# Optimization experiments

Hardware: AMD Instinct MI355X
Metric: run time of the kernel (lower is better)

Reference implementation:

```python
import jax, jax.numpy as jnp
import numpy as np

B, T, C, H = 4, 4096, 1024, 64


def setup_inputs() -> dict:
    key = jax.random.key(0)
    kx, kk, kq, kv = jax.random.split(key, 4)
    x = jax.random.normal(kx, (B, T, C), dtype=jnp.float32)
    # bias-free linear weights, stored as [in, out] so y = x @ W
    Wk = jax.random.normal(kk, (C, H), dtype=jnp.float32) * (C ** -0.5)
    Wq = jax.random.normal(kq, (C, H), dtype=jnp.float32) * (C ** -0.5)
    Wv = jax.random.normal(kv, (C, H), dtype=jnp.float32) * (C ** -0.5)
    return {"x": x, "Wk": Wk, "Wq": Wq, "Wv": Wv}


def reference(x, Wk, Wq, Wv):
    b, t, c = x.shape
    k = x @ Wk  # [B,T,H]
    q = x @ Wq
    v = x @ Wv
    # NOTE: original scales by C**-0.5 (num_embed), not head_size**-0.5
    wei = jnp.einsum('bqh,bkh->bqk', q, k) * (c ** -0.5)  # [B,T,T]
    causal = jnp.tril(jnp.ones((t, t), dtype=bool))
    wei = jnp.where(causal, wei, -jnp.inf)
    wei = jax.nn.softmax(wei, axis=-1)
    # dropout p=0.0 (eval) -> identity
    return jnp.einsum('bqk,bkh->bqh', wei, v)  # [B,T,H]
```

## Files before the change

### kernel.cpp

```cpp
#include <hip/hip_runtime.h>
#include <hip/hip_bf16.h>

typedef unsigned short u16;
typedef unsigned int u32;
using f32x4 = __attribute__((ext_vector_type(4))) float;
using s16x8 = __attribute__((ext_vector_type(8))) short;

#define BATCH 4
#define SEQ   4096
#define CDIM  1024
#define HDIM  64
#define QT_N  256

__device__ inline u16 f32_to_bf16(float f) {
    __bf16 h = (__bf16)f;
    return __builtin_bit_cast(u16, h);
}
__device__ inline u32 pkbf16(float a, float b) {
    return (u32)f32_to_bf16(a) | ((u32)f32_to_bf16(b) << 16);
}
__device__ inline f32x4 mfma16(s16x8 a, s16x8 b, f32x4 c) {
    return __builtin_amdgcn_mfma_f32_16x16x32_bf16(a, b, c, 0, 0, 0);
}


__global__ __launch_bounds__(64) void wtrans_kernel(
        const float* __restrict__ Wk, const float* __restrict__ Wq,
        const float* __restrict__ Wv, u16* __restrict__ Wtf) {
    int bx = blockIdx.x;
    int nt = bx >> 5, kc = bx & 31;
    int lane = threadIdx.x;
    int l16 = lane & 15, qd = lane >> 4;
    int n = nt * 16 + l16;
    int a = n >> 6, h = n & 63;
    const float* src = (a == 0) ? Wk : (a == 1) ? Wq : Wv;
    float scale = (a == 1) ? 0.045084220027780106f : 1.0f;
    u32 p[4];
#pragma unroll
    for (int pp = 0; pp < 4; ++pp) {
        int k = kc * 32 + qd * 8 + pp * 2;
        p[pp] = pkbf16(src[k * HDIM + h] * scale, src[(k + 1) * HDIM + h] * scale);
    }
    uint4 u; u.x = p[0]; u.y = p[1]; u.z = p[2]; u.w = p[3];
    *(uint4*)&Wtf[(size_t)((nt * 32 + kc) * 64 + lane) * 8] = u;
}

__global__ __launch_bounds__(512, 4) void proj_kernel(
        const float* __restrict__ x, const u16* __restrict__ Wtf,
        u16* __restrict__ qf, u16* __restrict__ kf, u16* __restrict__ vf) {
    __shared__ __align__(16) u16 xs[32][1032];
    int t = threadIdx.x, lane = t & 63, w = t >> 6;
    int quad = lane >> 4, l16 = lane & 15;
    int row0 = blockIdx.x * 32;

    const float* xb = x + (size_t)row0 * CDIM;
#pragma unroll 4
    for (int i = 0; i < 8; ++i) {
        int flat = i * 4096 + t * 8;
        float4 f0 = *(const float4*)(xb + flat);
        float4 f1 = *(const float4*)(xb + flat + 4);
        uint4 u;
        u.x = pkbf16(f0.x, f0.y); u.y = pkbf16(f0.z, f0.w);
        u.z = pkbf16(f1.x, f1.y); u.w = pkbf16(f1.z, f1.w);
        *(uint4*)&xs[flat >> 10][flat & 1023] = u;
    }
    __syncthreads();

    f32x4 acc[3];
#pragma unroll
    for (int n = 0; n < 3; ++n) acc[n] = (f32x4){0.f, 0.f, 0.f, 0.f};

    int nt_lo = (3 * w) >> 1;
    const u16* bp0 = Wtf + ((size_t)(nt_lo * 32) * 64 + lane) * 8;
    const u16* bp1 = bp0 + (size_t)32 * 64 * 8;

    if ((w & 1) == 0) {
#pragma unroll 4
        for (int kc = 0; kc < 32; ++kc) {
            s16x8 a0 = *(const s16x8*)&xs[l16][kc * 32 + quad * 8];
            s16x8 a1 = *(const s16x8*)&xs[16 + l16][kc * 32 + quad * 8];
            s16x8 b0 = *(const s16x8*)(bp0 + (size_t)kc * 512);
            s16x8 b1 = *(const s16x8*)(bp1 + (size_t)kc * 512);
            acc[0] = mfma16(a0, b0, acc[0]);
            acc[1] = mfma16(a1, b0, acc[1]);
            acc[2] = mfma16(a0, b1, acc[2]);
        }
    } else {
#pragma unroll 4
        for (int kc = 0; kc < 32; ++kc) {
            s16x8 a0 = *(const s16x8*)&xs[l16][kc * 32 + quad * 8];
            s16x8 a1 = *(const s16x8*)&xs[16 + l16][kc * 32 + quad * 8];
            s16x8 b0 = *(const s16x8*)(bp0 + (size_t)kc * 512);
            s16x8 b1 = *(const s16x8*)(bp1 + (size_t)kc * 512);
            acc[0] = mfma16(a1, b0, acc[0]);
            acc[1] = mfma16(a0, b1, acc[1]);
            acc[2] = mfma16(a1, b1, acc[2]);
        }
    }

#pragma unroll
    for (int i = 0; i < 3; ++i) {
        int u = 3 * w + i;
        int nt = u >> 1, rh = u & 1;
        int n0 = nt * 16;
        int rbase = row0 + rh * 16 + quad * 4;
        int bb = rbase >> 12, rl = rbase & 4095;
        if (n0 < 128) {
            u16* dst = (n0 < 64) ? kf : qf;
            int h = (n0 & 63) + l16;
            int tt16 = rl >> 4, hc = h >> 5, qd2 = (h >> 3) & 3, j = h & 7;
            size_t base = ((size_t)((bb * 256 + tt16) * 2 + hc) * 64
                           + qd2 * 16 + (rl & 15)) * 8 + j;
#pragma unroll
            for (int r = 0; r < 4; ++r)
                dst[base + (size_t)r * 8] = f32_to_bf16(acc[i][r]);
        } else {
            int ht = (n0 - 128) >> 4;
            int kc2 = rl >> 5, qdv = (rl >> 3) & 3, j0 = rl & 7;
            u32 lo = pkbf16(acc[i][0], acc[i][1]);
            u32 hi = pkbf16(acc[i][2], acc[i][3]);
            size_t base = ((size_t)((bb * 128 + kc2) * 4 + ht) * 64
                           + qdv * 16 + l16) * 8 + j0;
            uint2 u2; u2.x = lo; u2.y = hi;
            *(uint2*)&vf[base] = u2;
        }
    }
}

__global__ __launch_bounds__(512, 4) void flash_kernel(
        const u16* __restrict__ qf, const u16* __restrict__ kf,
        const u16* __restrict__ vf, float* __restrict__ out) {
    __shared__ float cb[8][32][68];
    __shared__ float lb[8][32];
    int t = threadIdx.x, w = t >> 6, lane = t & 63;
    int quad = lane >> 4, l16 = lane & 15;
    int bx = blockIdx.x;
    int b = bx & 3;
    int j = (bx & 255) >> 2;
    int qt2 = (bx < 256) ? (127 - j) : j;

    const u16* qp0 = qf + ((size_t)((b * QT_N + qt2 * 2) * 2) * 64 + lane) * 8;
    const u16* qp1 = qp0 + 2 * 64 * 8;
    s16x8 bq[2][2];
    bq[0][0] = *(const s16x8*)qp0;
    bq[0][1] = *(const s16x8*)(qp0 + 512);
    bq[1][0] = *(const s16x8*)qp1;
    bq[1][1] = *(const s16x8*)(qp1 + 512);
    s16x8 ones;
#pragma unroll
    for (int jj = 0; jj < 8; ++jj) ones[jj] = (short)0x3F80;

    f32x4 o[2][4], o5[2];
#pragma unroll
    for (int tl = 0; tl < 2; ++tl) {
        o5[tl] = (f32x4){0.f, 0.f, 0.f, 0.f};
#pragma unroll
        for (int i = 0; i < 4; ++i) o[tl][i] = (f32x4){0.f, 0.f, 0.f, 0.f};
    }

    int nb = (qt2 * 32 + 32 + 63) >> 6;
    int iters = (nb + 7) >> 3;
    int rowq0 = qt2 * 32 + l16;
    const u16* kfb = kf + (size_t)b * 256 * 2 * 512;
    const u16* vfb = vf + (size_t)b * 128 * 4 * 512;
    int a0 = ((quad & 1) * 32 + l16) * 4;
    int a1 = a0 + 64;
    bool lotile = (quad < 2);

    auto iteration = [&](int kb, bool domask) {
        f32x4 sT[2][4];
#pragma unroll
        for (int kt = 0; kt < 4; ++kt) {
            const u16* kp = kfb + ((size_t)((kb * 4 + kt) * 2) * 64 + lane) * 8;
            s16x8 k0 = *(const s16x8*)kp;
            s16x8 k1 = *(const s16x8*)(kp + 512);
            f32x4 z = (f32x4){0.f, 0.f, 0.f, 0.f};
            sT[0][kt] = mfma16(k1, bq[0][1], mfma16(k0, bq[0][0], z));
            sT[1][kt] = mfma16(k1, bq[1][1], mfma16(k0, bq[1][0], z));
        }
        u32 P01[2][4], P23[2][4];
#pragma unroll
        for (int tl = 0; tl < 2; ++tl) {
            int rowq = rowq0 + tl * 16;
#pragma unroll
            for (int kt = 0; kt < 4; ++kt) {
                float e[4];
#pragma unroll
                for (int r = 0; r < 4; ++r) {
                    float ev = __builtin_amdgcn_exp2f(sT[tl][kt][r]);
                    if (domask) {
                        int key = kb * 64 + kt * 16 + quad * 4 + r;
                        ev = (key > rowq) ? 0.f : ev;
                    }
                    e[r] = ev;
                }
                P01[tl][kt] = pkbf16(e[0], e[1]);
                P23[tl][kt] = pkbf16(e[2], e[3]);
            }
        }
#pragma unroll
        for (int c = 0; c < 2; ++c) {
            s16x8 vA[4];
#pragma unroll
            for (int ht = 0; ht < 4; ++ht)
                vA[ht] = *(const s16x8*)&vfb[((size_t)((kb * 2 + c) * 4 + ht) * 64
                                             + lane) * 8];
            int t0 = 2 * c, t1 = 2 * c + 1;
#pragma unroll
            for (int tl = 0; tl < 2; ++tl) {
                u32 x0 = (u32)__builtin_amdgcn_ds_bpermute(a0, (int)P01[tl][t0]);
                u32 y0 = (u32)__builtin_amdgcn_ds_bpermute(a0, (int)P01[tl][t1]);
                u32 x1 = (u32)__builtin_amdgcn_ds_bpermute(a0, (int)P23[tl][t0]);
                u32 y1 = (u32)__builtin_amdgcn_ds_bpermute(a0, (int)P23[tl][t1]);
                u32 x2 = (u32)__builtin_amdgcn_ds_bpermute(a1, (int)P01[tl][t0]);
                u32 y2 = (u32)__builtin_amdgcn_ds_bpermute(a1, (int)P01[tl][t1]);
                u32 x3 = (u32)__builtin_amdgcn_ds_bpermute(a1, (int)P23[tl][t0]);
                u32 y3 = (u32)__builtin_amdgcn_ds_bpermute(a1, (int)P23[tl][t1]);
                uint4 pu;
                pu.x = lotile ? x0 : y0;
                pu.y = lotile ? x1 : y1;
                pu.z = lotile ? x2 : y2;
                pu.w = lotile ? x3 : y3;
                s16x8 pb = __builtin_bit_cast(s16x8, pu);
#pragma unroll
                for (int ht = 0; ht < 4; ++ht)
                    o[tl][ht] = mfma16(vA[ht], pb, o[tl][ht]);
                o5[tl] = mfma16(ones, pb, o5[tl]);
            }
        }
    };

    for (int i = 0; i < iters - 1; ++i) iteration(8 * i + w, false);
    {
        int kb = 8 * (iters - 1) + w;
        if (kb < nb) iteration(kb, true);
    }
#pragma unroll
    for (int tl = 0; tl < 2; ++tl) {
#pragma unroll
        for (int ht = 0; ht < 4; ++ht)
#pragma unroll
            for (int r = 0; r < 4; ++r)
                cb[w][tl * 16 + l16][ht * 16 + quad * 4 + r] = o[tl][ht][r];
        if (quad == 0) lb[w][tl * 16 + l16] = o5[tl][0];
    }
    __syncthreads();
    int row = t >> 4, c0 = (t & 15) * 4;
    float l = 0.f;
    float4 s = (float4){0.f, 0.f, 0.f, 0.f};
#pragma unroll
    for (int w8 = 0; w8 < 8; ++w8) {
        l += lb[w8][row];
        float4 p = *(const float4*)&cb[w8][row][c0];
        s.x += p.x; s.y += p.y; s.z += p.z; s.w += p.w;
    }
    float rcp = 1.0f / l;
    s.x *= rcp; s.y *= rcp; s.z *= rcp; s.w *= rcp;
    *(float4*)&out[((size_t)(b * SEQ) + qt2 * 32 + row) * HDIM + c0] = s;
}

extern "C" void kernel_launch(void* const* d_in, const int* in_sizes, int n_in,
                              void* d_out, int out_size, void* d_ws, size_t ws_size,
                              hipStream_t stream) {
    const float* x  = (const float*)d_in[0];
    const float* Wk = (const float*)d_in[1];
    const float* Wq = (const float*)d_in[2];
    const float* Wv = (const float*)d_in[3];
    u16* wsu = (u16*)d_ws;
    u16* Wtf = wsu;
    u16* kf  = Wtf + 196608;
    u16* qf  = kf + 1048576;
    u16* vf  = qf + 1048576;
    float* out = (float*)d_out;

    hipLaunchKernelGGL(wtrans_kernel, dim3(384), dim3(64), 0, stream, Wk, Wq, Wv, Wtf);
    hipLaunchKernelGGL(proj_kernel, dim3(512), dim3(512), 0, stream, x, Wtf, qf, kf, vf);
    hipLaunchKernelGGL(flash_kernel, dim3((SEQ / 32) * BATCH), dim3(512), 0, stream,
                       qf, kf, vf, out);
}
```

Before: 125.4 us.

## Software-pipeline K tile loads and raise priority around PV MFMAs

Loads the next key block's K fragments into registers during the current iteration, after the score/exp stage, so global load latency overlaps with the PV MFMA work. The score computation and exp are interleaved per key tile rather than computed fully first. The PV MFMA group is wrapped in s_setprio to favour matrix issue across waves. This holds an extra 8 vector registers of K, which raises register pressure and could lower occupancy.

```diff
diff --git a/kernel.cpp b/kernel.cpp
--- a/kernel.cpp
+++ b/kernel.cpp
@@ -167,27 +167,33 @@
     int a1 = a0 + 64;
     bool lotile = (quad < 2);
 
-    auto iteration = [&](int kb, bool domask) {
-        f32x4 sT[2][4];
+    s16x8 kk[8];
+    auto loadK = [&](int kb) {
 #pragma unroll
         for (int kt = 0; kt < 4; ++kt) {
             const u16* kp = kfb + ((size_t)((kb * 4 + kt) * 2) * 64 + lane) * 8;
-            s16x8 k0 = *(const s16x8*)kp;
-            s16x8 k1 = *(const s16x8*)(kp + 512);
+            kk[2 * kt]     = *(const s16x8*)kp;
+            kk[2 * kt + 1] = *(const s16x8*)(kp + 512);
+        }
+    };
+
+    auto iteration = [&](int kb, int kbn, bool pref, bool domask) {
+        u32 P01[2][4], P23[2][4];
+#pragma unroll
+        for (int kt = 0; kt < 4; ++kt) {
             f32x4 z = (f32x4){0.f, 0.f, 0.f, 0.f};
-            sT[0][kt] = mfma16(k1, bq[0][1], mfma16(k0, bq[0][0], z));
-            sT[1][kt] = mfma16(k1, bq[1][1], mfma16(k0, bq[1][0], z));
-        }
-        u32 P01[2][4], P23[2][4];
-#pragma unroll
-        for (int tl = 0; tl < 2; ++tl) {
-            int rowq = rowq0 + tl * 16;
-#pragma unroll
-            for (int kt = 0; kt < 4; ++kt) {
+            f32x4 s0 = mfma16(kk[2 * kt + 1], bq[0][1],
+                              mfma16(kk[2 * kt], bq[0][0], z));
+            f32x4 s1 = mfma16(kk[2 * kt + 1], bq[1][1],
+                              mfma16(kk[2 * kt], bq[1][0], z));
+#pragma unroll
+            for (int tl = 0; tl < 2; ++tl) {
+                f32x4 sv = tl ? s1 : s0;
+                int rowq = rowq0 + tl * 16;
                 float e[4];
 #pragma unroll
                 for (int r = 0; r < 4; ++r) {
-                    float ev = __builtin_amdgcn_exp2f(sT[tl][kt][r]);
+                    float ev = __builtin_amdgcn_exp2f(sv[r]);
                     if (domask) {
                         int key = kb * 64 + kt * 16 + quad * 4 + r;
                         ev = (key > rowq) ? 0.f : ev;
@@ -198,6 +204,7 @@
                 P23[tl][kt] = pkbf16(e[2], e[3]);
             }
         }
+        if (pref) loadK(kbn);
 #pragma unroll
         for (int c = 0; c < 2; ++c) {
             s16x8 vA[4];
@@ -222,18 +229,25 @@
                 pu.z = lotile ? x2 : y2;
                 pu.w = lotile ? x3 : y3;
                 s16x8 pb = __builtin_bit_cast(s16x8, pu);
+                __builtin_amdgcn_s_setprio(1);
 #pragma unroll
                 for (int ht = 0; ht < 4; ++ht)
                     o[tl][ht] = mfma16(vA[ht], pb, o[tl][ht]);
                 o5[tl] = mfma16(ones, pb, o5[tl]);
+                __builtin_amdgcn_s_setprio(0);
             }
         }
     };
 
-    for (int i = 0; i < iters - 1; ++i) iteration(8 * i + w, false);
+    loadK(w);
+    for (int i = 0; i < iters - 1; ++i) {
+        int kb = 8 * i + w;
+        int kbn = kb + 8; if (kbn > 63) kbn = 63;
+        iteration(kb, kbn, true, false);
+    }
     {
         int kb = 8 * (iters - 1) + w;
-        if (kb < nb) iteration(kb, true);
+        if (kb < nb) iteration(kb, kb, false, true);
     }
 #pragma unroll
     for (int tl = 0; tl < 2; ++tl) {
```

Result: slower. 145.4 us (+16.0%).
